# Optimization experiments

Measured on AMD Instinct MI355X. Metric: run time of the kernel, lower is better.

Reference implementation:

```python
import jax, jax.numpy as jnp
import numpy as np

TWO_PI = 2.0 * np.pi

def ringify(x):
    # wrap values to [-pi, pi)
    return (x + np.pi) % TWO_PI - np.pi

def complex_mean(x, axes):
    # circular mean direction: atan2(sum sin, sum ringify(cos))
    dir_x = ringify(jnp.cos(x)).sum(axis=axes)
    dir_y = jnp.sin(x).sum(axis=axes)
    return jnp.arctan2(dir_y, dir_x)

def setup_inputs() -> dict:
    key = jax.random.key(0)
    k1, k2, k3, k4 = jax.random.split(key, 4)
    B = 4096
    return {
        "x": jax.random.normal(k1, (B, 1, 28, 28), dtype=jnp.float32),
        "conv1_w": jax.random.normal(k2, (4, 1, 2, 2), dtype=jnp.float32),
        "conv2_w": jax.random.normal(k3, (8, 4, 4, 4), dtype=jnp.float32),
        "ff_w": jax.random.normal(k4, (288, 10), dtype=jnp.float32),
    }

def reference(x, conv1_w, conv2_w, ff_w):
    B = x.shape[0]
    x = ringify(x).reshape(B, 1, 28, 28)

    # --- ring conv1: 2x2 kernel, stride 2 (non-overlapping patches) ---
    # [B,1,28,28] -> [B,14,14,1,2,2]  (matches unfold(2,2,2).unfold(3,2,2).permute)
    p1 = x.reshape(B, 1, 14, 2, 14, 2).transpose(0, 2, 4, 1, 3, 5)
    w1 = conv1_w.transpose(1, 2, 3, 0)            # [1,2,2,4]
    d1 = ringify(p1[..., None] - w1)              # [B,14,14,1,2,2,4]
    h1 = complex_mean(d1, (3, 4, 5))              # [B,14,14,4]

    # --- ring conv2: 4x4 kernel, stride 2 (overlapping patches) ---
    h1 = h1.transpose(0, 3, 1, 2)                 # [B,4,14,14]
    idx = (jnp.arange(6) * 2)[:, None] + jnp.arange(4)[None, :]  # [6,4] window rows/cols
    p2 = h1[:, :, idx, :][:, :, :, :, idx]        # [B,4,6,4,6,4]
    p2 = p2.transpose(0, 2, 4, 1, 3, 5)           # [B,6,6,4,4,4]
    w2 = conv2_w.transpose(1, 2, 3, 0)            # [4,4,4,8]
    d2 = ringify(p2[..., None] - w2)              # [B,6,6,4,4,4,8]
    h2 = complex_mean(d2, (3, 4, 5))              # [B,6,6,8]

    # --- ring feed-forward ---
    f = h2.reshape(B, 288)
    d3 = ringify(f[:, :, None] - ff_w)            # [B,288,10]
    out = complex_mean(d3, (1,))                  # [B,10]
    return jnp.sin(out)
```

## Files before the change

kernel.cpp:

```cpp
#include <hip/hip_runtime.h>
#include <math.h>

#define B_PER_BLK 2

__global__ __launch_bounds__(640) void ringnn_kernel(
    const float* __restrict__ x,
    const float* __restrict__ w1g,
    const float* __restrict__ w2g,
    const float* __restrict__ ffg,
    float* __restrict__ out)
{
    __shared__ float2 trig1[16];
    __shared__ float2 trig2[520];
    __shared__ float2 sc1[B_PER_BLK * 1008];
    __shared__ float2 sc2[B_PER_BLK * 288];
    const int tid = threadIdx.x;

    if (tid < 16) {
        float s, c; __sincosf(w1g[tid], &s, &c);
        trig1[tid] = make_float2(c, s);
    }
    if (tid < 512) {
        int oc = tid >> 6, e = tid & 63;
        float s, c; __sincosf(w2g[tid], &s, &c);
        trig2[(oc >> 1) * 130 + e * 2 + (oc & 1)] = make_float2(c, s);
    }
    __syncthreads();

    if (tid < 392) {
        int img = tid / 196, pos = tid % 196;
        int i = pos / 14, j = pos % 14;
        const float* xb = x + ((size_t)blockIdx.x * B_PER_BLK + img) * 784;
        float2 r0 = *(const float2*)(xb + (2 * i) * 28 + 2 * j);
        float2 r1 = *(const float2*)(xb + (2 * i + 1) * 28 + 2 * j);
        float sx[4], cx[4];
        __sincosf(r0.x, &sx[0], &cx[0]);
        __sincosf(r0.y, &sx[1], &cx[1]);
        __sincosf(r1.x, &sx[2], &cx[2]);
        __sincosf(r1.y, &sx[3], &cx[3]);
        #pragma unroll
        for (int oc = 0; oc < 4; oc++) {
            float4 wa = *(const float4*)(&trig1[oc * 4]);
            float4 wb = *(const float4*)(&trig1[oc * 4 + 2]);
            float Y = 0.f, X = 0.f;
            Y = fmaf(sx[0], wa.x, fmaf(-cx[0], wa.y, Y));
            X = fmaf(cx[0], wa.x, fmaf( sx[0], wa.y, X));
            Y = fmaf(sx[1], wa.z, fmaf(-cx[1], wa.w, Y));
            X = fmaf(cx[1], wa.z, fmaf( sx[1], wa.w, X));
            Y = fmaf(sx[2], wb.x, fmaf(-cx[2], wb.y, Y));
            X = fmaf(cx[2], wb.x, fmaf( sx[2], wb.y, X));
            Y = fmaf(sx[3], wb.z, fmaf(-cx[3], wb.w, Y));
            X = fmaf(cx[3], wb.z, fmaf( sx[3], wb.w, X));
            float inv = rsqrtf(fmaxf(fmaf(X, X, Y * Y), 1e-30f));
            sc1[img * 1008 + oc * 252 + i * 18 + j] = make_float2(Y * inv, X * inv);
        }
    }
    __syncthreads();

    if (tid < 192) {
        int img = tid / 96, r = tid % 96;
        int oi = r >> 4, ojg = (r >> 3) & 1, ocp = (r >> 1) & 3, hf = r & 1;
        const float2* scb = sc1 + img * 1008;
        const float2* wbp = trig2 + ocp * 130;
        float aY[3][2] = {{0.f,0.f},{0.f,0.f},{0.f,0.f}};
        float aX[3][2] = {{0.f,0.f},{0.f,0.f},{0.f,0.f}};
        #pragma unroll
        for (int ch = 0; ch < 4; ch++) {
            #pragma unroll
            for (int kk = 0; kk < 2; kk++) {
                int ki = hf * 2 + kk;
                int base = ch * 252 + (oi * 2 + ki) * 18 + ojg * 6;
                float4 f0 = *(const float4*)(scb + base);
                float4 f1 = *(const float4*)(scb + base + 2);
                float4 f2 = *(const float4*)(scb + base + 4);
                float4 f3 = *(const float4*)(scb + base + 6);
                float ss[8] = {f0.x,f0.z,f1.x,f1.z,f2.x,f2.z,f3.x,f3.z};
                float cc[8] = {f0.y,f0.w,f1.y,f1.w,f2.y,f2.w,f3.y,f3.w};
                int e0 = ch * 16 + ki * 4;
                #pragma unroll
                for (int kj = 0; kj < 4; kj++) {
                    float4 wv = *(const float4*)(wbp + (e0 + kj) * 2);
                    #pragma unroll
                    for (int ojl = 0; ojl < 3; ojl++) {
                        float s = ss[ojl * 2 + kj], c = cc[ojl * 2 + kj];
                        aY[ojl][0] = fmaf(s, wv.x, fmaf(-c, wv.y, aY[ojl][0]));
                        aX[ojl][0] = fmaf(c, wv.x, fmaf( s, wv.y, aX[ojl][0]));
                        aY[ojl][1] = fmaf(s, wv.z, fmaf(-c, wv.w, aY[ojl][1]));
                        aX[ojl][1] = fmaf(c, wv.z, fmaf( s, wv.w, aX[ojl][1]));
                    }
                }
            }
        }
        #pragma unroll
        for (int ojl = 0; ojl < 3; ojl++) {
            float y0 = aY[ojl][0]; y0 += __shfl_xor(y0, 1);
            float y1 = aY[ojl][1]; y1 += __shfl_xor(y1, 1);
            float x0 = aX[ojl][0]; x0 += __shfl_xor(x0, 1);
            float x1 = aX[ojl][1]; x1 += __shfl_xor(x1, 1);
            float Y = hf ? y1 : y0;
            float X = hf ? x1 : x0;
            float inv = rsqrtf(fmaxf(fmaf(X, X, Y * Y), 1e-30f));
            int p = oi * 6 + ojg * 3 + ojl;
            sc2[img * 288 + p * 8 + ocp * 2 + hf] = make_float2(Y * inv, X * inv);
        }
    }
    __syncthreads();

    if (tid < 320) {
        int img = tid / 160, r = tid % 160;
        int n = r >> 4, s = r & 15;
        const float2* scb = sc2 + img * 288;
        float Y = 0.f, X = 0.f;
        #pragma unroll
        for (int i = 0; i < 18; i++) {
            int k = s * 18 + i;
            float2 sc = scb[k];
            float ws_, wc_;
            __sincosf(ffg[k * 10 + n], &ws_, &wc_);
            Y = fmaf(sc.x, wc_, fmaf(-sc.y, ws_, Y));
            X = fmaf(sc.y, wc_, fmaf( sc.x, ws_, X));
        }
        #pragma unroll
        for (int off = 1; off < 16; off <<= 1) {
            Y += __shfl_xor(Y, off);
            X += __shfl_xor(X, off);
        }
        if (s == 0) {
            size_t b = (size_t)blockIdx.x * B_PER_BLK + img;
            out[b * 10 + n] = Y * rsqrtf(fmaxf(fmaf(X, X, Y * Y), 1e-30f));
        }
    }
}

extern "C" void kernel_launch(void* const* d_in, const int* in_sizes, int n_in,
                              void* d_out, int out_size, void* d_ws, size_t ws_size,
                              hipStream_t stream) {
    const float* x  = (const float*)d_in[0];
    const float* w1 = (const float*)d_in[1];
    const float* w2 = (const float*)d_in[2];
    const float* ff = (const float*)d_in[3];
    float* out = (float*)d_out;
    const int B = in_sizes[0] / 784;
    ringnn_kernel<<<B / B_PER_BLK, 640, 0, stream>>>(x, w1, w2, ff, out);
}
```

Baseline: 91.13 us.

## Precompute feed-forward weight sin/cos once in a separate kernel and widen FF stage

Adds a small pre-kernel that computes cos/sin of the 2880 feed-forward weights once per call into the workspace, transposed to [n][k] layout, instead of each block recomputing sincos per weight. The FF stage now uses all 640 threads (32 lanes per output) with strided coalesced reads and a shuffle-down reduction. Shared arrays get explicit 16-byte alignment. It adds a second kernel launch and a global read of the trig table per block.

```diff
diff --git a/kernel.cpp b/kernel.cpp
--- a/kernel.cpp
+++ b/kernel.cpp
@@ -2,18 +2,29 @@
 #include <math.h>
 
 #define B_PER_BLK 2
+#define NFF 2880
+
+__global__ void precompute_fft(const float* __restrict__ ff,
+                               float2* __restrict__ out) {
+    int idx = blockIdx.x * blockDim.x + threadIdx.x;
+    if (idx < NFF) {
+        int k = idx / 10, n = idx % 10;
+        float s, c; sincosf(ff[idx], &s, &c);
+        out[n * 288 + k] = make_float2(c, s);
+    }
+}
 
 __global__ __launch_bounds__(640) void ringnn_kernel(
     const float* __restrict__ x,
     const float* __restrict__ w1g,
     const float* __restrict__ w2g,
-    const float* __restrict__ ffg,
+    const float2* __restrict__ fft,
     float* __restrict__ out)
 {
-    __shared__ float2 trig1[16];
-    __shared__ float2 trig2[520];
-    __shared__ float2 sc1[B_PER_BLK * 1008];
-    __shared__ float2 sc2[B_PER_BLK * 288];
+    __shared__ __align__(16) float2 trig1[16];
+    __shared__ __align__(16) float2 trig2[520];
+    __shared__ __align__(16) float2 sc1[B_PER_BLK * 1008];
+    __shared__ __align__(16) float2 sc2[B_PER_BLK * 288];
     const int tid = threadIdx.x;
 
     if (tid < 16) {
@@ -70,10 +81,10 @@
             for (int kk = 0; kk < 2; kk++) {
                 int ki = hf * 2 + kk;
                 int base = ch * 252 + (oi * 2 + ki) * 18 + ojg * 6;
-                float4 f0 = *(const float4*)(scb + base);
-                float4 f1 = *(const float4*)(scb + base + 2);
-                float4 f2 = *(const float4*)(scb + base + 4);
-                float4 f3 = *(const float4*)(scb + base + 6);
+                float4 f0 = *(const float4*)(sc1 + img * 1008 + base);
+                float4 f1 = *(const float4*)(sc1 + img * 1008 + base + 2);
+                float4 f2 = *(const float4*)(sc1 + img * 1008 + base + 4);
+                float4 f3 = *(const float4*)(sc1 + img * 1008 + base + 6);
                 float ss[8] = {f0.x,f0.z,f1.x,f1.z,f2.x,f2.z,f3.x,f3.z};
                 float cc[8] = {f0.y,f0.w,f1.y,f1.w,f2.y,f2.w,f3.y,f3.w};
                 int e0 = ch * 16 + ki * 4;
@@ -106,24 +117,24 @@
     }
     __syncthreads();
 
-    if (tid < 320) {
-        int img = tid / 160, r = tid % 160;
-        int n = r >> 4, s = r & 15;
+    {
+        int img = tid / 320, r = tid % 320;
+        int n = r >> 5, s = r & 31;
         const float2* scb = sc2 + img * 288;
+        const float2* wn = fft + n * 288;
         float Y = 0.f, X = 0.f;
         #pragma unroll
-        for (int i = 0; i < 18; i++) {
-            int k = s * 18 + i;
+        for (int i = 0; i < 9; i++) {
+            int k = i * 32 + s;
             float2 sc = scb[k];
-            float ws_, wc_;
-            __sincosf(ffg[k * 10 + n], &ws_, &wc_);
-            Y = fmaf(sc.x, wc_, fmaf(-sc.y, ws_, Y));
-            X = fmaf(sc.y, wc_, fmaf( sc.x, ws_, X));
+            float2 w = wn[k];
+            Y = fmaf(sc.x, w.x, fmaf(-sc.y, w.y, Y));
+            X = fmaf(sc.y, w.x, fmaf( sc.x, w.y, X));
         }
         #pragma unroll
-        for (int off = 1; off < 16; off <<= 1) {
-            Y += __shfl_xor(Y, off);
-            X += __shfl_xor(X, off);
+        for (int off = 16; off > 0; off >>= 1) {
+            Y += __shfl_down(Y, off, 32);
+            X += __shfl_down(X, off, 32);
         }
         if (s == 0) {
             size_t b = (size_t)blockIdx.x * B_PER_BLK + img;
@@ -141,5 +152,8 @@
     const float* ff = (const float*)d_in[3];
     float* out = (float*)d_out;
     const int B = in_sizes[0] / 784;
-    ringnn_kernel<<<B / B_PER_BLK, 640, 0, stream>>>(x, w1, w2, ff, out);
+
+    float2* fft = (float2*)d_ws;
+    precompute_fft<<<(NFF + 255) / 256, 256, 0, stream>>>(ff, fft);
+    ringnn_kernel<<<B / B_PER_BLK, 640, 0, stream>>>(x, w1, w2, fft, out);
 }
```

Result: no change. 89.56 us (-1.7%).
